# Kernel optimization log

Hardware: AMD Instinct MI355X
Metric: run time of the kernel (lower is better)

Reference implementation:

```python
import jax, jax.numpy as jnp
import numpy as np

# Config mirrors module init: C=12 channels, include_time=True -> d=13, depth=3
# sig_channels = d + d^2 + d^3 = 2379

def setup_inputs() -> dict:
    key = jax.random.key(0)
    k1, k2, k3 = jax.random.split(key, 3)
    N, C, J, T, L = 8, 12, 25, 64, 5
    d = C + 1
    sig_channels = d + d * d + d ** 3  # 2379
    out_dim = 256
    x = jax.random.normal(k1, (N, C, J, T, L), dtype=jnp.float32)
    W = jax.random.normal(k2, (out_dim, sig_channels), dtype=jnp.float32) / np.sqrt(sig_channels)
    b = jax.random.normal(k3, (out_dim,), dtype=jnp.float32) * 0.01
    return {"x": x, "W": W, "b": b}


def _signature_depth3(path):
    """Truncated (depth 3) path signature with zero basepoint.
    path: [B, L, d] -> sig: [B, d + d^2 + d^3]
    Chen's identity: s <- s * exp(dx), with exp(dx)_n = dx^{(x)n} / n!
    """
    B, L, d = path.shape
    # basepoint=True: prepend zeros, then take increments
    inc = jnp.diff(jnp.concatenate([jnp.zeros((B, 1, d), path.dtype), path], axis=1), axis=1)  # [B, L, d]

    def step(carry, dx):
        s1, s2, s3 = carry  # [B,d], [B,d*d], [B,d^3]
        e2 = 0.5 * jnp.einsum('bi,bj->bij', dx, dx)                     # [B,d,d]
        e3 = (jnp.einsum('bij,bk->bijk', e2, dx) / 3.0).reshape(B, d ** 3)  # dx^3/6
        n1 = s1 + dx
        n2 = s2 + jnp.einsum('bi,bj->bij', s1, dx).reshape(B, d * d) + e2.reshape(B, d * d)
        n3 = (s3
              + jnp.einsum('bij,bk->bijk', s2.reshape(B, d, d), dx).reshape(B, d ** 3)
              + jnp.einsum('bi,bjk->bijk', s1, e2).reshape(B, d ** 3)
              + e3)
        return (n1, n2, n3), None

    init = (jnp.zeros((B, d), path.dtype),
            jnp.zeros((B, d * d), path.dtype),
            jnp.zeros((B, d ** 3), path.dtype))
    (s1, s2, s3), _ = jax.lax.scan(step, init, jnp.moveaxis(inc, 1, 0))
    return jnp.concatenate([s1, s2, s3], axis=-1)


def reference(x, W, b):
    N, C, J, T, L = x.shape
    B = J * T * N
    # windowed gather: block (i*T+j)*N..(..+1)*N = x[:,:,i,j,:].permute(0,2,1)
    path = jnp.transpose(x, (2, 3, 0, 4, 1)).reshape(B, L, C)  # [J*T*N, L, C]
    # Augment include_time=True: append time channel linspace(0,1,L)
    t = jnp.linspace(0.0, 1.0, L, dtype=path.dtype)
    path = jnp.concatenate([path, jnp.broadcast_to(t[None, :, None], (B, L, 1))], axis=-1)
    sig = _signature_depth3(path)                 # [B, 2379]
    z = sig @ W.T + b                             # [B, out_dim]
    # scatter back: res[:, :, i, j] = z[(i*T+j)*N : ...]
    return jnp.transpose(z.reshape(J, T, N, -1), (2, 3, 0, 1))  # [N, out_dim, J, T]
```

## Files before the change

### kernel.cpp

```cpp
#include <hip/hip_runtime.h>
#include <hip/hip_bf16.h>

typedef float f32x4 __attribute__((ext_vector_type(4)));
typedef short s16x8 __attribute__((ext_vector_type(8)));

#define SIGC 2379
#define KPAD 2432
#define NKT  76
#define SROW 2440
#define NPATH 12800


__device__ inline void split2(float v, __hip_bfloat16* h, __hip_bfloat16* l) {
    __hip_bfloat16 hh = __float2bfloat16(v);
    *h = hh;
    *l = __float2bfloat16(v - __bfloat162float(hh));
}

__device__ inline void gload_lds16(const __hip_bfloat16* g, __hip_bfloat16* l) {
    __builtin_amdgcn_global_load_lds(
        (const __attribute__((address_space(1))) void*)g,
        (__attribute__((address_space(3))) void*)l,
        16, 0, 0);
}

__global__ __launch_bounds__(256) void wconv_kernel(const float* __restrict__ W,
                                                    __hip_bfloat16* __restrict__ Wh,
                                                    __hip_bfloat16* __restrict__ Wl)
{
    int k = blockIdx.x * 256 + threadIdx.x;
    int n = blockIdx.y;
    if (k >= KPAD) return;
    float v = (k < SIGC) ? W[(size_t)n * SIGC + k] : 0.0f;
    size_t off = ((size_t)(n >> 4) * NKT + (k >> 5)) * 512 + ((k >> 3) & 3) * 128 + (n & 15) * 8 + (k & 7);
    split2(v, &Wh[off], &Wl[off]);
}

__global__ __launch_bounds__(256) void sig_kernel(const float* __restrict__ x,
                                                  __hip_bfloat16* __restrict__ Ah,
                                                  __hip_bfloat16* __restrict__ Al_,
                                                  int r_start)
{
    __shared__ float inc_s[4][5][16];
    __shared__ __align__(16) __hip_bfloat16 hi_s[4][SROW];
    __shared__ __align__(16) __hip_bfloat16 lo_s[4][SROW];

    const int t = threadIdx.x;
    const int w = t >> 6;
    const int lane = t & 63;

    const int p0 = lane;
    const int p1 = lane + 64;
    const int p2 = lane + 128;
    const bool has2 = (p2 < 169);
    const int i0 = p0 / 13, j0 = p0 - i0 * 13;
    const int i1 = p1 / 13, j1 = p1 - i1 * 13;
    const int i2 = p2 / 13, j2 = p2 - i2 * 13;

    for (int pp = 0; pp < 4; ++pp) {
        const int r = r_start + blockIdx.x * 16 + pp * 4 + w;
        const int nn = r & 7;
        const int jj = (r >> 3) & 63;
        const int ii = r >> 9;

        __syncthreads();
        if (lane < 13) {
            if (lane < 12) {
                const float* px = x + ((size_t)(nn * 12 + lane) * 1600 + ii * 64 + jj) * 5;
                float prev = 0.0f;
                #pragma unroll
                for (int l = 0; l < 5; ++l) {
                    float v = px[l];
                    inc_s[w][l][lane] = v - prev;
                    prev = v;
                }
            } else {
                inc_s[w][0][12] = 0.0f;
                #pragma unroll
                for (int l = 1; l < 5; ++l) inc_s[w][l][12] = 0.25f;
            }
        }
        __syncthreads();

        float s1i0 = 0.0f, s1i1 = 0.0f, s1i2 = 0.0f;
        float s2p0 = 0.0f, s2p1 = 0.0f, s2p2 = 0.0f;
        float s1own = 0.0f;
        float s3a[13], s3b[13], s3c[13];
        #pragma unroll
        for (int k = 0; k < 13; ++k) { s3a[k] = 0.0f; s3b[k] = 0.0f; s3c[k] = 0.0f; }

        for (int l = 0; l < 5; ++l) {
            float dxl[13];
            #pragma unroll
            for (int k = 0; k < 13; ++k) dxl[k] = inc_s[w][l][k];

            {
                float dxi = inc_s[w][l][i0];
                float dxj = inc_s[w][l][j0];
                float C   = s2p0 + 0.5f * dxj * (s1i0 + dxi * (1.0f / 3.0f));
                #pragma unroll
                for (int k = 0; k < 13; ++k) s3a[k] += dxl[k] * C;
                s2p0 += s1i0 * dxj + 0.5f * dxi * dxj;
                s1i0 += dxi;
            }
            {
                float dxi = inc_s[w][l][i1];
                float dxj = inc_s[w][l][j1];
                float C   = s2p1 + 0.5f * dxj * (s1i1 + dxi * (1.0f / 3.0f));
                #pragma unroll
                for (int k = 0; k < 13; ++k) s3b[k] += dxl[k] * C;
                s2p1 += s1i1 * dxj + 0.5f * dxi * dxj;
                s1i1 += dxi;
            }
            if (has2) {
                float dxi = inc_s[w][l][i2];
                float dxj = inc_s[w][l][j2];
                float C   = s2p2 + 0.5f * dxj * (s1i2 + dxi * (1.0f / 3.0f));
                #pragma unroll
                for (int k = 0; k < 13; ++k) s3c[k] += dxl[k] * C;
                s2p2 += s1i2 * dxj + 0.5f * dxi * dxj;
                s1i2 += dxi;
            }
            if (lane < 13) s1own += inc_s[w][l][lane];
        }

        if (lane < 13) split2(s1own, &hi_s[w][lane], &lo_s[w][lane]);
        split2(s2p0, &hi_s[w][13 + p0], &lo_s[w][13 + p0]);
        split2(s2p1, &hi_s[w][13 + p1], &lo_s[w][13 + p1]);
        if (has2) split2(s2p2, &hi_s[w][13 + p2], &lo_s[w][13 + p2]);
        #pragma unroll
        for (int k = 0; k < 13; ++k) split2(s3a[k], &hi_s[w][182 + p0 * 13 + k], &lo_s[w][182 + p0 * 13 + k]);
        #pragma unroll
        for (int k = 0; k < 13; ++k) split2(s3b[k], &hi_s[w][182 + p1 * 13 + k], &lo_s[w][182 + p1 * 13 + k]);
        if (has2) {
            #pragma unroll
            for (int k = 0; k < 13; ++k) split2(s3c[k], &hi_s[w][182 + p2 * 13 + k], &lo_s[w][182 + p2 * 13 + k]);
        }
        if (lane < KPAD - SIGC) {
            hi_s[w][SIGC + lane] = __float2bfloat16(0.0f);
            lo_s[w][SIGC + lane] = __float2bfloat16(0.0f);
        }

        __syncthreads();

        const int rtl = blockIdx.x;
        const int rr = t & 3, ks = (t >> 2) & 3, ts = t >> 4;
        #pragma unroll
        for (int it2 = 0; it2 < 5; ++it2) {
            int kt = it2 * 16 + ts;
            if (kt < NKT) {
                size_t off = ((size_t)rtl * NKT + kt) * 512 + ks * 128 + (pp * 4 + rr) * 8;
                int lidx = kt * 32 + ks * 8;
                *reinterpret_cast<int4*>(Ah + off)  = *reinterpret_cast<const int4*>(&hi_s[rr][lidx]);
                *reinterpret_cast<int4*>(Al_ + off) = *reinterpret_cast<const int4*>(&lo_s[rr][lidx]);
            }
        }
    }
}

__global__ __launch_bounds__(256) void gemm_kernel(const __hip_bfloat16* __restrict__ Ah,
                                                   const __hip_bfloat16* __restrict__ Al_,
                                                   const __hip_bfloat16* __restrict__ Wh,
                                                   const __hip_bfloat16* __restrict__ Wl,
                                                   const float* __restrict__ b,
                                                   float* __restrict__ out,
                                                   int r_start, int nmblk)
{
    __shared__ __align__(16) __hip_bfloat16 L[2][24 * 512];

    const int bid = blockIdx.x;
    const int x8 = bid & 7, h = (bid >> 3) & 1, q = bid >> 4;
    const int mIdx = q * 8 + x8;
    if (mIdx >= nmblk) return;

    const int t = threadIdx.x;
    const int lane = t & 63;
    const int w = t >> 6;
    const int wm = w >> 1, wn = w & 1;
    const int n0 = h * 128;
    const int rt0 = mIdx * 4;
    const int nt0 = h * 8;

    f32x4 acc[2][4] = {};

    auto stage = [&](int buf, int kt) {
        #pragma unroll
        for (int s = 0; s < 6; ++s) {
            int tt = w * 6 + s;
            const __hip_bfloat16* g;
            if (tt < 4)       g = Ah  + ((size_t)(rt0 + tt)      * NKT + kt) * 512;
            else if (tt < 8)  g = Al_ + ((size_t)(rt0 + tt - 4)  * NKT + kt) * 512;
            else if (tt < 16) g = Wh  + ((size_t)(nt0 + tt - 8)  * NKT + kt) * 512;
            else              g = Wl  + ((size_t)(nt0 + tt - 16) * NKT + kt) * 512;
            gload_lds16(g + lane * 8, &L[buf][tt * 512]);
        }
    };

    stage(0, 0);
    int cur = 0;
    __syncthreads();

    for (int kt = 0; kt < NKT; ++kt) {
        if (kt + 1 < NKT) stage(cur ^ 1, kt + 1);

        const int fb = (lane >> 4) * 128 + (lane & 15) * 8;
        s16x8 ah[2], al4[2], bh[4], bl4[4];
        #pragma unroll
        for (int mm = 0; mm < 2; ++mm) {
            int base = (2 * wm + mm) * 512 + fb;
            ah[mm]  = *reinterpret_cast<const s16x8*>(&L[cur][base]);
            al4[mm] = *reinterpret_cast<const s16x8*>(&L[cur][2048 + base]);
        }
        #pragma unroll
        for (int nnn = 0; nnn < 4; ++nnn) {
            int base = (4 * wn + nnn) * 512 + fb;
            bh[nnn]  = *reinterpret_cast<const s16x8*>(&L[cur][4096 + base]);
            bl4[nnn] = *reinterpret_cast<const s16x8*>(&L[cur][8192 + base]);
        }

        #pragma unroll
        for (int mm = 0; mm < 2; ++mm)
            #pragma unroll
            for (int nnn = 0; nnn < 4; ++nnn) {
                acc[mm][nnn] = __builtin_amdgcn_mfma_f32_16x16x32_bf16(ah[mm],  bh[nnn],  acc[mm][nnn], 0, 0, 0);
                acc[mm][nnn] = __builtin_amdgcn_mfma_f32_16x16x32_bf16(ah[mm],  bl4[nnn], acc[mm][nnn], 0, 0, 0);
                acc[mm][nnn] = __builtin_amdgcn_mfma_f32_16x16x32_bf16(al4[mm], bh[nnn],  acc[mm][nnn], 0, 0, 0);
            }

        __syncthreads();
        cur ^= 1;
    }

    float* T = (float*)&L[0][0];
    #pragma unroll
    for (int mm = 0; mm < 2; ++mm)
        #pragma unroll
        for (int nnn = 0; nnn < 4; ++nnn)
            #pragma unroll
            for (int rr = 0; rr < 4; ++rr) {
                int p = wm * 32 + mm * 16 + (lane >> 4) * 4 + rr;
                int o = wn * 64 + nnn * 16 + (lane & 15);
                T[p * 132 + o] = acc[mm][nnn][rr];
            }
    __syncthreads();

    const int pbase = r_start + mIdx * 64;
    const int ii = pbase >> 9;
    const int jj0 = (pbase >> 3) & 63;
    const int ol = t >> 1, hh = t & 1;
    const int o = n0 + ol;
    const float bo = b[o];
    #pragma unroll
    for (int c = 0; c < 4; ++c) {
        int ni = hh * 4 + c;
        float v[8];
        #pragma unroll
        for (int qq = 0; qq < 8; ++qq) v[qq] = T[(qq * 8 + ni) * 132 + ol] + bo;
        float* dst = out + (size_t)(ni * 256 + o) * 1600 + ii * 64 + jj0;
        *reinterpret_cast<float4*>(dst)     = make_float4(v[0], v[1], v[2], v[3]);
        *reinterpret_cast<float4*>(dst + 4) = make_float4(v[4], v[5], v[6], v[7]);
    }
}

extern "C" void kernel_launch(void* const* d_in, const int* in_sizes, int n_in,
                              void* d_out, int out_size, void* d_ws, size_t ws_size,
                              hipStream_t stream)
{
    const float* x = (const float*)d_in[0];
    const float* W = (const float*)d_in[1];
    const float* b = (const float*)d_in[2];
    float* out = (float*)d_out;

    char* ws = (char*)d_ws;
    __hip_bfloat16* Wh = (__hip_bfloat16*)ws;
    __hip_bfloat16* Wl = Wh + (size_t)16 * NKT * 512;
    size_t a_off = (((size_t)16 * NKT * 512 * 2 * 2) + 255) & ~(size_t)255;

    size_t avail = (ws_size > a_off) ? ws_size - a_off : 0;
    long long maxp = (long long)(avail / ((size_t)KPAD * 2 * 2));
    int chunk = (int)((maxp / 128) * 128);
    if (chunk > NPATH) chunk = NPATH;
    if (chunk < 128) chunk = 128;

    __hip_bfloat16* Ah = (__hip_bfloat16*)(ws + a_off);
    __hip_bfloat16* Al_ = Ah + (size_t)chunk * KPAD;

    wconv_kernel<<<dim3(10, 256), 256, 0, stream>>>(W, Wh, Wl);

    for (int r0 = 0; r0 < NPATH; r0 += chunk) {
        int cnt = NPATH - r0;
        if (cnt > chunk) cnt = chunk;
        int nmblk = cnt / 64;
        int nblk = ((nmblk + 7) / 8) * 16;
        sig_kernel<<<dim3(cnt / 16), 256, 0, stream>>>(x, Ah, Al_, r0);
        gemm_kernel<<<dim3(nblk), 256, 0, stream>>>(Ah, Al_, Wh, Wl, b, out, r0, nmblk);
    }
}
```

Before: 105.2 us.

## Split GEMM over K into two halves with narrower N tiles and separate reduce kernel

The GEMM now tiles output columns 64 wide instead of 128 and splits the K loop into two halves. This gives eight blocks per 64-row M tile instead of two, which raises parallelism across the GPU. Partial sums go to a new fp32 workspace buffer, and a separate reduce kernel adds the two halves plus bias before doing the transposed scatter. The cost is extra global traffic for the partials, an additional kernel launch, and more re-reading of the A tiles across N blocks.

```diff
diff --git a/kernel.cpp b/kernel.cpp
--- a/kernel.cpp
+++ b/kernel.cpp
@@ -7,6 +7,7 @@
 #define SIGC 2379
 #define KPAD 2432
 #define NKT  76
+#define NKT_HALF 38
 #define SROW 2440
 #define NPATH 12800
 
@@ -162,49 +163,49 @@
                                                    const __hip_bfloat16* __restrict__ Al_,
                                                    const __hip_bfloat16* __restrict__ Wh,
                                                    const __hip_bfloat16* __restrict__ Wl,
-                                                   const float* __restrict__ b,
-                                                   float* __restrict__ out,
-                                                   int r_start, int nmblk)
-{
-    __shared__ __align__(16) __hip_bfloat16 L[2][24 * 512];
+                                                   float* __restrict__ P,
+                                                   int chunk_alloc)
+{
+    __shared__ __align__(16) __hip_bfloat16 L[2][16 * 512];
 
     const int bid = blockIdx.x;
-    const int x8 = bid & 7, h = (bid >> 3) & 1, q = bid >> 4;
-    const int mIdx = q * 8 + x8;
-    if (mIdx >= nmblk) return;
+    const int mIdx = bid >> 3;
+    const int s = bid & 7;
+    const int n2 = s & 3;
+    const int ksp = s >> 2;
 
     const int t = threadIdx.x;
     const int lane = t & 63;
     const int w = t >> 6;
     const int wm = w >> 1, wn = w & 1;
-    const int n0 = h * 128;
     const int rt0 = mIdx * 4;
-    const int nt0 = h * 8;
-
-    f32x4 acc[2][4] = {};
+    const int nt0 = n2 * 4;
+    const int kt0 = ksp * NKT_HALF;
+
+    f32x4 acc[2][2] = {};
 
     auto stage = [&](int buf, int kt) {
         #pragma unroll
-        for (int s = 0; s < 6; ++s) {
-            int tt = w * 6 + s;
+        for (int s2 = 0; s2 < 4; ++s2) {
+            int tt = w * 4 + s2;
             const __hip_bfloat16* g;
             if (tt < 4)       g = Ah  + ((size_t)(rt0 + tt)      * NKT + kt) * 512;
             else if (tt < 8)  g = Al_ + ((size_t)(rt0 + tt - 4)  * NKT + kt) * 512;
-            else if (tt < 16) g = Wh  + ((size_t)(nt0 + tt - 8)  * NKT + kt) * 512;
-            else              g = Wl  + ((size_t)(nt0 + tt - 16) * NKT + kt) * 512;
+            else if (tt < 12) g = Wh  + ((size_t)(nt0 + tt - 8)  * NKT + kt) * 512;
+            else              g = Wl  + ((size_t)(nt0 + tt - 12) * NKT + kt) * 512;
             gload_lds16(g + lane * 8, &L[buf][tt * 512]);
         }
     };
 
-    stage(0, 0);
+    stage(0, kt0);
     int cur = 0;
     __syncthreads();
 
-    for (int kt = 0; kt < NKT; ++kt) {
-        if (kt + 1 < NKT) stage(cur ^ 1, kt + 1);
+    for (int kk = 0; kk < NKT_HALF; ++kk) {
+        if (kk + 1 < NKT_HALF) stage(cur ^ 1, kt0 + kk + 1);
 
         const int fb = (lane >> 4) * 128 + (lane & 15) * 8;
-        s16x8 ah[2], al4[2], bh[4], bl4[4];
+        s16x8 ah[2], al4[2], bh[2], bl4[2];
         #pragma unroll
         for (int mm = 0; mm < 2; ++mm) {
             int base = (2 * wm + mm) * 512 + fb;
@@ -212,53 +213,71 @@
             al4[mm] = *reinterpret_cast<const s16x8*>(&L[cur][2048 + base]);
         }
         #pragma unroll
-        for (int nnn = 0; nnn < 4; ++nnn) {
-            int base = (4 * wn + nnn) * 512 + fb;
-            bh[nnn]  = *reinterpret_cast<const s16x8*>(&L[cur][4096 + base]);
-            bl4[nnn] = *reinterpret_cast<const s16x8*>(&L[cur][8192 + base]);
+        for (int nn = 0; nn < 2; ++nn) {
+            int base = (8 + 2 * wn + nn) * 512 + fb;
+            bh[nn]  = *reinterpret_cast<const s16x8*>(&L[cur][base]);
+            bl4[nn] = *reinterpret_cast<const s16x8*>(&L[cur][2048 + base]);
         }
 
         #pragma unroll
         for (int mm = 0; mm < 2; ++mm)
             #pragma unroll
-            for (int nnn = 0; nnn < 4; ++nnn) {
-                acc[mm][nnn] = __builtin_amdgcn_mfma_f32_16x16x32_bf16(ah[mm],  bh[nnn],  acc[mm][nnn], 0, 0, 0);
-                acc[mm][nnn] = __builtin_amdgcn_mfma_f32_16x16x32_bf16(ah[mm],  bl4[nnn], acc[mm][nnn], 0, 0, 0);
-                acc[mm][nnn] = __builtin_amdgcn_mfma_f32_16x16x32_bf16(al4[mm], bh[nnn],  acc[mm][nnn], 0, 0, 0);
+            for (int nn = 0; nn < 2; ++nn) {
+                acc[mm][nn] = __builtin_amdgcn_mfma_f32_16x16x32_bf16(ah[mm],  bh[nn],  acc[mm][nn], 0, 0, 0);
+                acc[mm][nn] = __builtin_amdgcn_mfma_f32_16x16x32_bf16(ah[mm],  bl4[nn], acc[mm][nn], 0, 0, 0);
+                acc[mm][nn] = __builtin_amdgcn_mfma_f32_16x16x32_bf16(al4[mm], bh[nn],  acc[mm][nn], 0, 0, 0);
             }
 
         __syncthreads();
         cur ^= 1;
     }
 
-    float* T = (float*)&L[0][0];
+    float* Pb = P + ((size_t)ksp * chunk_alloc + mIdx * 64) * 256 + n2 * 64;
     #pragma unroll
     for (int mm = 0; mm < 2; ++mm)
         #pragma unroll
-        for (int nnn = 0; nnn < 4; ++nnn)
+        for (int nn = 0; nn < 2; ++nn) {
+            int o = wn * 32 + nn * 16 + (lane & 15);
             #pragma unroll
             for (int rr = 0; rr < 4; ++rr) {
                 int p = wm * 32 + mm * 16 + (lane >> 4) * 4 + rr;
-                int o = wn * 64 + nnn * 16 + (lane & 15);
-                T[p * 132 + o] = acc[mm][nnn][rr];
-            }
-    __syncthreads();
-
-    const int pbase = r_start + mIdx * 64;
+                Pb[(size_t)p * 256 + o] = acc[mm][nn][rr];
+            }
+        }
+}
+
+__global__ __launch_bounds__(256) void reduce_kernel(const float* __restrict__ P,
+                                                     const float* __restrict__ b,
+                                                     float* __restrict__ out,
+                                                     int chunk_alloc, int r_start)
+{
+    const int mb = blockIdx.x;
+    const int pbase = r_start + mb * 64;
     const int ii = pbase >> 9;
     const int jj0 = (pbase >> 3) & 63;
+    const int t = threadIdx.x;
     const int ol = t >> 1, hh = t & 1;
-    const int o = n0 + ol;
-    const float bo = b[o];
+
+    const float* P0 = P + (size_t)mb * 64 * 256;
+    const float* P1 = P0 + (size_t)chunk_alloc * 256;
+
     #pragma unroll
-    for (int c = 0; c < 4; ++c) {
-        int ni = hh * 4 + c;
-        float v[8];
-        #pragma unroll
-        for (int qq = 0; qq < 8; ++qq) v[qq] = T[(qq * 8 + ni) * 132 + ol] + bo;
-        float* dst = out + (size_t)(ni * 256 + o) * 1600 + ii * 64 + jj0;
-        *reinterpret_cast<float4*>(dst)     = make_float4(v[0], v[1], v[2], v[3]);
-        *reinterpret_cast<float4*>(dst + 4) = make_float4(v[4], v[5], v[6], v[7]);
+    for (int oh = 0; oh < 2; ++oh) {
+        int o = oh * 128 + ol;
+        float bo = b[o];
+        #pragma unroll
+        for (int c = 0; c < 4; ++c) {
+            int ni = hh * 4 + c;
+            float v[8];
+            #pragma unroll
+            for (int qq = 0; qq < 8; ++qq) {
+                size_t idx = (size_t)(qq * 8 + ni) * 256 + o;
+                v[qq] = P0[idx] + P1[idx] + bo;
+            }
+            float* dst = out + (size_t)(ni * 256 + o) * 1600 + ii * 64 + jj0;
+            *reinterpret_cast<float4*>(dst)     = make_float4(v[0], v[1], v[2], v[3]);
+            *reinterpret_cast<float4*>(dst + 4) = make_float4(v[4], v[5], v[6], v[7]);
+        }
     }
 }
 
@@ -277,22 +296,22 @@
     size_t a_off = (((size_t)16 * NKT * 512 * 2 * 2) + 255) & ~(size_t)255;
 
     size_t avail = (ws_size > a_off) ? ws_size - a_off : 0;
-    long long maxp = (long long)(avail / ((size_t)KPAD * 2 * 2));
-    int chunk = (int)((maxp / 128) * 128);
+    long long maxp = (long long)(avail / ((size_t)KPAD * 4 + 2048));
+    int chunk = (int)((maxp / 64) * 64);
     if (chunk > NPATH) chunk = NPATH;
-    if (chunk < 128) chunk = 128;
+    if (chunk < 64) chunk = 64;
 
     __hip_bfloat16* Ah = (__hip_bfloat16*)(ws + a_off);
     __hip_bfloat16* Al_ = Ah + (size_t)chunk * KPAD;
+    float* P = (float*)(Al_ + (size_t)chunk * KPAD);
 
     wconv_kernel<<<dim3(10, 256), 256, 0, stream>>>(W, Wh, Wl);
 
     for (int r0 = 0; r0 < NPATH; r0 += chunk) {
         int cnt = NPATH - r0;
         if (cnt > chunk) cnt = chunk;
-        int nmblk = cnt / 64;
-        int nblk = ((nmblk + 7) / 8) * 16;
         sig_kernel<<<dim3(cnt / 16), 256, 0, stream>>>(x, Ah, Al_, r0);
-        gemm_kernel<<<dim3(nblk), 256, 0, stream>>>(Ah, Al_, Wh, Wl, b, out, r0, nmblk);
+        gemm_kernel<<<dim3((cnt / 64) * 8), 256, 0, stream>>>(Ah, Al_, Wh, Wl, P, chunk);
+        reduce_kernel<<<dim3(cnt / 64), 256, 0, stream>>>(P, b, out, chunk, r0);
     }
 }
```

Result: slower. 137.6 us (+30.8%).
